# Kernel optimization log

Measured on AMD Instinct MI355X. Metric: run time of the kernel, lower is better.

Reference implementation:

```python
import jax, jax.numpy as jnp
import numpy as np

B, N, E, C_IN, C_OUT = 4, 50000, 800000, 128, 128


def setup_inputs() -> dict:
    key = jax.random.key(0)
    k1, k2, k3, k4, k5 = jax.random.split(key, 5)
    x = jax.random.normal(k1, (B, N, C_IN), dtype=jnp.float32)
    edge_row = jax.random.randint(k2, (E,), 0, N, dtype=jnp.int32)
    edge_col = jax.random.randint(k3, (E,), 0, N, dtype=jnp.int32)
    edge_vals = jax.random.uniform(k4, (E,), dtype=jnp.float32)
    W = jax.random.normal(k5, (C_IN, C_OUT), dtype=jnp.float32) * 0.1  # weight_stddev=0.1
    b = jnp.full((C_OUT,), 0.1, dtype=jnp.float32)  # bias_constant=0.1
    return {"x": x, "edge_row": edge_row, "edge_col": edge_col,
            "edge_vals": edge_vals, "W": W, "b": b}


def reference(x, edge_row, edge_col, edge_vals, W, b):
    # Sparse adjacency aggregation: agg[b, r, :] = sum_e vals[e] * x[b, col[e], :]
    n = x.shape[1]

    def spmm(xb):  # xb: [N, C_in]
        msgs = xb[edge_col] * edge_vals[:, None]          # [E, C_in]
        return jax.ops.segment_sum(msgs, edge_row, num_segments=n)  # [N, C_in]

    agg = jax.vmap(spmm)(x)                               # [B, N, C_in]
    out = jnp.einsum('bnc,co->bno', agg, W) + b           # dense GEMM + bias
    return jax.nn.relu(out)
```

## Files before the change

### kernel.cpp

```cpp
#include <hip/hip_runtime.h>

#define NROWS 50000
#define BATCH 4
#define CH    128
#define CAP   64

typedef float  f32x4  __attribute__((ext_vector_type(4)));
typedef __bf16 bf16x8 __attribute__((ext_vector_type(8)));
typedef short  s16x8  __attribute__((ext_vector_type(8)));

static __device__ __forceinline__ unsigned short f2bf(float f) {
    unsigned u = __builtin_bit_cast(unsigned, f);
    u += 0x7fffu + ((u >> 16) & 1u);
    return (unsigned short)(u >> 16);
}

__global__ void k_zero(int* __restrict__ cnt, int n) {
    int i = blockIdx.x * blockDim.x + threadIdx.x;
    if (i < n) cnt[i] = 0;
}

__global__ void k_scatter(const int* __restrict__ row, const int* __restrict__ col,
                          const float* __restrict__ vals, int E,
                          int* __restrict__ cnt,
                          int* __restrict__ cols_p, float* __restrict__ vals_p) {
    int e = blockIdx.x * blockDim.x + threadIdx.x;
    if (e < E) {
        int r = row[e];
        int p = atomicAdd(&cnt[r], 1);
        if (p < CAP) {
            cols_p[r * CAP + p] = col[e];
            vals_p[r * CAP + p] = vals[e];
        }
    }
}

__global__ __launch_bounds__(256) void k_xw(const float* __restrict__ x,
                                            const float* __restrict__ W,
                                            unsigned short* __restrict__ y) {
    __shared__ unsigned short WtL[128 * 136];
    const int tid = threadIdx.x;
    for (int idx = tid; idx < 128 * 128; idx += 256) {
        int k = idx >> 7, n = idx & 127;
        WtL[n * 136 + k] = f2bf(W[idx]);
    }
    __syncthreads();

    const int wave = tid >> 6;
    const int lane = tid & 63;
    const int m    = lane & 15;
    const int quad = lane >> 4;

    const int NSTRIP = (BATCH * NROWS) / 64;
    for (int s = blockIdx.x; s < NSTRIP; s += gridDim.x) {
        const int row0 = s * 64 + wave * 16;

        s16x8 a_s[4];
        const float* xr = x + (size_t)(row0 + m) * CH;
        #pragma unroll
        for (int kk = 0; kk < 4; ++kk) {
            const float4* p = (const float4*)(xr + kk * 32 + quad * 8);
            float4 f0 = p[0], f1 = p[1];
            s16x8 sv;
            sv[0] = f2bf(f0.x); sv[1] = f2bf(f0.y); sv[2] = f2bf(f0.z); sv[3] = f2bf(f0.w);
            sv[4] = f2bf(f1.x); sv[5] = f2bf(f1.y); sv[6] = f2bf(f1.z); sv[7] = f2bf(f1.w);
            a_s[kk] = sv;
        }

        #pragma unroll
        for (int nt = 0; nt < 8; ++nt) {
            f32x4 acc = {0.f, 0.f, 0.f, 0.f};
            #pragma unroll
            for (int kk = 0; kk < 4; ++kk) {
                bf16x8 b = *(const bf16x8*)&WtL[(nt * 16 + m) * 136 + kk * 32 + quad * 8];
                acc = __builtin_amdgcn_mfma_f32_16x16x32_bf16(
                          __builtin_bit_cast(bf16x8, a_s[kk]), b, acc, 0, 0, 0);
            }
            #pragma unroll
            for (int reg = 0; reg < 4; ++reg) {
                int i  = row0 + quad * 4 + reg;
                int bb = i / NROWS;
                int n  = i - bb * NROWS;
                y[((size_t)n * BATCH + bb) * CH + nt * 16 + m] = f2bf(acc[reg]);
            }
        }
    }
}

__global__ __launch_bounds__(256) void k_spmm2(const unsigned* __restrict__ y,
                                               const int* __restrict__ cnt,
                                               const int* __restrict__ cols_p,
                                               const float* __restrict__ vals_p,
                                               const float* __restrict__ bias,
                                               float* __restrict__ out) {
    __shared__ int   lcol[CAP];
    __shared__ float lval[CAP];
    const int r    = blockIdx.x;
    const int tid  = threadIdx.x;
    const int b    = tid >> 6;
    const int lane = tid & 63;
    const int deg  = min(cnt[r], CAP);
    if (tid < deg) {
        lcol[tid] = cols_p[r * CAP + tid];
        lval[tid] = vals_p[r * CAP + tid];
    }
    __syncthreads();

    const unsigned* __restrict__ Y = y + b * (CH / 2) + lane;
    float ax = 0.f, ay = 0.f;
    int e = 0;
    for (; e + 8 <= deg; e += 8) {
        int   c[8];
        float v[8];
        unsigned u[8];
        #pragma unroll
        for (int j = 0; j < 8; ++j) { c[j] = lcol[e + j]; v[j] = lval[e + j]; }
        #pragma unroll
        for (int j = 0; j < 8; ++j) u[j] = Y[(size_t)c[j] * 256];
        #pragma unroll
        for (int j = 0; j < 8; ++j) {
            ax += v[j] * __builtin_bit_cast(float, u[j] << 16);
            ay += v[j] * __builtin_bit_cast(float, u[j] & 0xffff0000u);
        }
    }
    for (; e < deg; ++e) {
        int   cc = lcol[e];
        float v  = lval[e];
        unsigned u = Y[(size_t)cc * 256];
        ax += v * __builtin_bit_cast(float, u << 16);
        ay += v * __builtin_bit_cast(float, u & 0xffff0000u);
    }

    float2 bv = ((const float2*)bias)[lane];
    float2 o;
    o.x = fmaxf(ax + bv.x, 0.f);
    o.y = fmaxf(ay + bv.y, 0.f);
    ((float2*)(out + ((size_t)b * NROWS + r) * CH))[lane] = o;
}

extern "C" void kernel_launch(void* const* d_in, const int* in_sizes, int n_in,
                              void* d_out, int out_size, void* d_ws, size_t ws_size,
                              hipStream_t stream) {
    const float* x        = (const float*)d_in[0];
    const int*   edge_row = (const int*)d_in[1];
    const int*   edge_col = (const int*)d_in[2];
    const float* edge_val = (const float*)d_in[3];
    const float* W        = (const float*)d_in[4];
    const float* bias     = (const float*)d_in[5];
    float*       out      = (float*)d_out;

    const int E = in_sizes[1];

    int*            cnt    = (int*)d_ws;
    int*            cols_p = cnt + 50048;
    float*          vals_p = (float*)(cols_p + NROWS * CAP);
    unsigned short* y      = (unsigned short*)(vals_p + NROWS * CAP);

    k_zero<<<(NROWS + 255) / 256, 256, 0, stream>>>(cnt, NROWS);
    k_scatter<<<(E + 255) / 256, 256, 0, stream>>>(edge_row, edge_col, edge_val, E,
                                                   cnt, cols_p, vals_p);
    k_xw<<<625, 256, 0, stream>>>(x, W, y);
    k_spmm2<<<NROWS, 256, 0, stream>>>((const unsigned*)y, cnt, cols_p, vals_p,
                                       bias, out);
}
```

Measured before the change: 379.1 us.

## Pack CSR col/val into 64-bit entries and coalesce XW output via LDS

The scatter kernel now stores column and value as one packed 64-bit entry, so the SpMM kernel loads a single array into shared memory instead of two. The XW GEMM stages its bf16 output tile in per-wave shared memory and writes full 16-byte row segments, replacing the scattered 2-byte stores. The XW grid is doubled. Together these cut store transactions and halve the CSR fetch count, at the cost of extra LDS per block, which may reduce occupancy.

```diff
diff --git a/kernel.cpp b/kernel.cpp
--- a/kernel.cpp
+++ b/kernel.cpp
@@ -22,15 +22,16 @@
 
 __global__ void k_scatter(const int* __restrict__ row, const int* __restrict__ col,
                           const float* __restrict__ vals, int E,
-                          int* __restrict__ cnt,
-                          int* __restrict__ cols_p, float* __restrict__ vals_p) {
+                          int* __restrict__ cnt, unsigned long long* __restrict__ csr) {
     int e = blockIdx.x * blockDim.x + threadIdx.x;
     if (e < E) {
         int r = row[e];
         int p = atomicAdd(&cnt[r], 1);
         if (p < CAP) {
-            cols_p[r * CAP + p] = col[e];
-            vals_p[r * CAP + p] = vals[e];
+            unsigned long long pk =
+                (unsigned long long)(unsigned)col[e] |
+                ((unsigned long long)__builtin_bit_cast(unsigned, vals[e]) << 32);
+            csr[r * CAP + p] = pk;
         }
     }
 }
@@ -39,6 +40,7 @@
                                             const float* __restrict__ W,
                                             unsigned short* __restrict__ y) {
     __shared__ unsigned short WtL[128 * 136];
+    __shared__ unsigned short yt[4][16 * 136];
     const int tid = threadIdx.x;
     for (int idx = tid; idx < 128 * 128; idx += 256) {
         int k = idx >> 7, n = idx & 127;
@@ -50,6 +52,7 @@
     const int lane = tid & 63;
     const int m    = lane & 15;
     const int quad = lane >> 4;
+    unsigned short* __restrict__ myt = yt[wave];
 
     const int NSTRIP = (BATCH * NROWS) / 64;
     for (int s = blockIdx.x; s < NSTRIP; s += gridDim.x) {
@@ -77,56 +80,58 @@
                           __builtin_bit_cast(bf16x8, a_s[kk]), b, acc, 0, 0, 0);
             }
             #pragma unroll
-            for (int reg = 0; reg < 4; ++reg) {
-                int i  = row0 + quad * 4 + reg;
-                int bb = i / NROWS;
-                int n  = i - bb * NROWS;
-                y[((size_t)n * BATCH + bb) * CH + nt * 16 + m] = f2bf(acc[reg]);
-            }
+            for (int reg = 0; reg < 4; ++reg)
+                myt[(quad * 4 + reg) * 136 + nt * 16 + m] = f2bf(acc[reg]);
+        }
+
+        #pragma unroll
+        for (int it = 0; it < 4; ++it) {
+            const int lrow = it * 4 + (lane >> 4);
+            const int seg  = lane & 15;
+            uint4 v = *(const uint4*)&myt[lrow * 136 + seg * 8];
+            const int i  = row0 + lrow;
+            const int bb = i / NROWS;
+            const int n  = i - bb * NROWS;
+            *(uint4*)&y[((size_t)n * BATCH + bb) * CH + seg * 8] = v;
         }
     }
 }
 
 __global__ __launch_bounds__(256) void k_spmm2(const unsigned* __restrict__ y,
                                                const int* __restrict__ cnt,
-                                               const int* __restrict__ cols_p,
-                                               const float* __restrict__ vals_p,
+                                               const unsigned long long* __restrict__ csr,
                                                const float* __restrict__ bias,
                                                float* __restrict__ out) {
-    __shared__ int   lcol[CAP];
-    __shared__ float lval[CAP];
+    __shared__ unsigned long long lcsr[CAP];
     const int r    = blockIdx.x;
     const int tid  = threadIdx.x;
     const int b    = tid >> 6;
     const int lane = tid & 63;
     const int deg  = min(cnt[r], CAP);
-    if (tid < deg) {
-        lcol[tid] = cols_p[r * CAP + tid];
-        lval[tid] = vals_p[r * CAP + tid];
-    }
+    if (tid < deg) lcsr[tid] = csr[r * CAP + tid];
     __syncthreads();
 
     const unsigned* __restrict__ Y = y + b * (CH / 2) + lane;
     float ax = 0.f, ay = 0.f;
     int e = 0;
     for (; e + 8 <= deg; e += 8) {
-        int   c[8];
-        float v[8];
+        unsigned long long pk[8];
         unsigned u[8];
         #pragma unroll
-        for (int j = 0; j < 8; ++j) { c[j] = lcol[e + j]; v[j] = lval[e + j]; }
+        for (int j = 0; j < 8; ++j) pk[j] = lcsr[e + j];
         #pragma unroll
-        for (int j = 0; j < 8; ++j) u[j] = Y[(size_t)c[j] * 256];
+        for (int j = 0; j < 8; ++j) u[j] = Y[(size_t)(unsigned)pk[j] * 256];
         #pragma unroll
         for (int j = 0; j < 8; ++j) {
-            ax += v[j] * __builtin_bit_cast(float, u[j] << 16);
-            ay += v[j] * __builtin_bit_cast(float, u[j] & 0xffff0000u);
+            float v = __builtin_bit_cast(float, (unsigned)(pk[j] >> 32));
+            ax += v * __builtin_bit_cast(float, u[j] << 16);
+            ay += v * __builtin_bit_cast(float, u[j] & 0xffff0000u);
         }
     }
     for (; e < deg; ++e) {
-        int   cc = lcol[e];
-        float v  = lval[e];
-        unsigned u = Y[(size_t)cc * 256];
+        unsigned long long pk = lcsr[e];
+        float v = __builtin_bit_cast(float, (unsigned)(pk >> 32));
+        unsigned u = Y[(size_t)(unsigned)pk * 256];
         ax += v * __builtin_bit_cast(float, u << 16);
         ay += v * __builtin_bit_cast(float, u & 0xffff0000u);
     }
@@ -151,15 +156,13 @@
 
     const int E = in_sizes[1];
 
-    int*            cnt    = (int*)d_ws;
-    int*            cols_p = cnt + 50048;
-    float*          vals_p = (float*)(cols_p + NROWS * CAP);
-    unsigned short* y      = (unsigned short*)(vals_p + NROWS * CAP);
+    int*                cnt = (int*)d_ws;
+    unsigned long long* csr = (unsigned long long*)(cnt + 50048);
+    unsigned short*     y   = (unsigned short*)(csr + (size_t)NROWS * CAP);
 
     k_zero<<<(NROWS + 255) / 256, 256, 0, stream>>>(cnt, NROWS);
     k_scatter<<<(E + 255) / 256, 256, 0, stream>>>(edge_row, edge_col, edge_val, E,
-                                                   cnt, cols_p, vals_p);
-    k_xw<<<625, 256, 0, stream>>>(x, W, y);
-    k_spmm2<<<NROWS, 256, 0, stream>>>((const unsigned*)y, cnt, cols_p, vals_p,
-                                       bias, out);
+                                                   cnt, csr);
+    k_xw<<<1250, 256, 0, stream>>>(x, W, y);
+    k_spmm2<<<NROWS, 256, 0, stream>>>((const unsigned*)y, cnt, csr, bias, out);
 }
```

Result: faster. 364.2 us (-4.0%).
